# Optimization experiments

Measured on AMD Instinct MI355X. Metric: run time of the kernel, lower is better.

The kernel has to match this reference:

```python
import jax, jax.numpy as jnp
import numpy as np

B, T, N, H, DK = 4, 16, 256, 8, 64

def setup_inputs() -> dict:
    key = jax.random.key(0)
    k1, k2, k3 = jax.random.split(key, 3)
    queries = jax.random.normal(k1, (B, T, N, H, DK), dtype=jnp.float32)
    keys = jax.random.normal(k2, (B, T, N, H, DK), dtype=jnp.float32)
    values = jax.random.normal(k3, (B, T, N, H, DK), dtype=jnp.float32)
    attention_mask = jnp.zeros((B, T, 1, N, N), dtype=bool)  # unused: mask_flag=False
    return {"queries": queries, "keys": keys, "values": values, "attention_mask": attention_mask}

def reference(queries, keys, values, attention_mask):
    # queries: B T N H d_k; keys/values: B T S H d_k/d_v
    d_k = queries.shape[-1]
    scale = 1.0 / jnp.sqrt(jnp.asarray(d_k, queries.dtype))
    # scores: B T H N S
    scores = jnp.einsum('btnhe,btshe->bthns', queries, keys)
    # mask_flag=False -> no masking; dropout is identity in eval mode
    A = jax.nn.softmax(scale * scores, axis=-1)
    V = jnp.einsum('bthns,btshd->btnhd', A, values)
    return V
```

## Files before the change

kernel.cpp:

```cpp
#include <hip/hip_runtime.h>


typedef short short8 __attribute__((ext_vector_type(8)));
typedef float floatx4 __attribute__((ext_vector_type(4)));

__device__ __forceinline__ unsigned cvt_pk(float lo, float hi) {
  unsigned r;
  asm("v_cvt_pk_bf16_f32 %0, %1, %2" : "=v"(r) : "v"(lo), "v"(hi));
  return r;
}

constexpr int KSTR = 72;
constexpr int VSTR = 264;

__global__ __launch_bounds__(512, 4) void attn_kernel(
    const float* __restrict__ Q, const float* __restrict__ K,
    const float* __restrict__ V, float* __restrict__ O) {
  __shared__ __align__(16) short Klds[256 * KSTR];
  __shared__ __align__(16) short Vt[64 * VSTR];

  const int inst = blockIdx.x;
  const int h    = inst & 7;
  const int bt   = inst >> 3;
  const int base = bt * (256 * 512) + h * 64;
  const int tid  = threadIdx.x;

  {
    const float* Kb = K + base;
    #pragma unroll
    for (int i = 0; i < 8; ++i) {
      int idx = i * 512 + tid;
      int s = idx >> 4, c4 = idx & 15;
      float4 v = *reinterpret_cast<const float4*>(Kb + s * 512 + c4 * 4);
      uint2 w;
      w.x = cvt_pk(v.x, v.y);
      w.y = cvt_pk(v.z, v.w);
      *reinterpret_cast<uint2*>(&Klds[s * KSTR + c4 * 4]) = w;
    }
  }
  {
    const float* Vb = V + base;
    unsigned* Vt32 = reinterpret_cast<unsigned*>(Vt);
    #pragma unroll
    for (int i = 0; i < 4; ++i) {
      int idx = i * 512 + tid;
      int sp = idx >> 4, c4 = idx & 15;
      int s = sp * 2;
      float4 v0 = *reinterpret_cast<const float4*>(Vb + s * 512 + c4 * 4);
      float4 v1 = *reinterpret_cast<const float4*>(Vb + (s + 1) * 512 + c4 * 4);
      #pragma unroll
      for (int k = 0; k < 4; ++k) {
        Vt32[(c4 * 4 + k) * (VSTR / 2) + sp] = cvt_pk((&v0.x)[k], (&v1.x)[k]);
      }
    }
  }

  const int wave  = tid >> 6;
  const int lane  = tid & 63;
  const int c     = lane & 15;
  const int g     = lane >> 4;
  const int ghalf = (g & 1) * 32;
  const int gsel  = g >> 1;

  const float SCQ = 0.125f * 1.4426950408889634f;
  short8 qf[2][2];
  #pragma unroll
  for (int pass = 0; pass < 2; ++pass) {
    #pragma unroll
    for (int ks2 = 0; ks2 < 2; ++ks2) {
      const float* qp =
          Q + base + (pass * 128 + wave * 16 + c) * 512 + ks2 * 32 + g * 8;
      float4 a = *reinterpret_cast<const float4*>(qp);
      float4 b = *reinterpret_cast<const float4*>(qp + 4);
      union { unsigned u[4]; short8 s; } t;
      t.u[0] = cvt_pk(a.x * SCQ, a.y * SCQ);
      t.u[1] = cvt_pk(a.z * SCQ, a.w * SCQ);
      t.u[2] = cvt_pk(b.x * SCQ, b.y * SCQ);
      t.u[3] = cvt_pk(b.z * SCQ, b.w * SCQ);
      qf[pass][ks2] = t.s;
    }
  }
  __syncthreads();

  #pragma unroll
  for (int pass = 0; pass < 2; ++pass) {
    const int n0 = pass * 128 + wave * 16;

    floatx4 ao[4];
    #pragma unroll
    for (int dt = 0; dt < 4; ++dt) ao[dt] = floatx4{0.f, 0.f, 0.f, 0.f};
    float ps0 = 0.f, ps1 = 0.f, ps2 = 0.f, ps3 = 0.f;

    #pragma unroll
    for (int ks = 0; ks < 8; ++ks) {
      unsigned pk2[2][2];
      #pragma unroll
      for (int tt = 0; tt < 2; ++tt) {
        const int t = 2 * ks + tt;
        floatx4 acc = {0.f, 0.f, 0.f, 0.f};
        #pragma unroll
        for (int ks2 = 0; ks2 < 2; ++ks2) {
          short8 kf = *reinterpret_cast<const short8*>(
              &Klds[(t * 16 + c) * KSTR + ks2 * 32 + g * 8]);
          acc = __builtin_amdgcn_mfma_f32_16x16x32_bf16(kf, qf[pass][ks2], acc,
                                                        0, 0, 0);
        }
        float e0 = exp2f(acc[0]);
        float e1 = exp2f(acc[1]);
        float e2 = exp2f(acc[2]);
        float e3 = exp2f(acc[3]);
        ps0 += e0; ps1 += e1; ps2 += e2; ps3 += e3;
        pk2[tt][0] = cvt_pk(e0, e1);
        pk2[tt][1] = cvt_pk(e2, e3);
      }

      unsigned a0 = __shfl(pk2[0][0], ghalf + c);
      unsigned a1 = __shfl(pk2[0][1], ghalf + c);
      unsigned a2 = __shfl(pk2[0][0], ghalf + 16 + c);
      unsigned a3 = __shfl(pk2[0][1], ghalf + 16 + c);
      unsigned b0 = __shfl(pk2[1][0], ghalf + c);
      unsigned b1 = __shfl(pk2[1][1], ghalf + c);
      unsigned b2 = __shfl(pk2[1][0], ghalf + 16 + c);
      unsigned b3 = __shfl(pk2[1][1], ghalf + 16 + c);
      union { unsigned u[4]; short8 s; } pa;
      pa.u[0] = gsel ? b0 : a0;
      pa.u[1] = gsel ? b1 : a1;
      pa.u[2] = gsel ? b2 : a2;
      pa.u[3] = gsel ? b3 : a3;

      #pragma unroll
      for (int dt = 0; dt < 4; ++dt) {
        short8 vf = *reinterpret_cast<const short8*>(
            &Vt[(dt * 16 + c) * VSTR + ks * 32 + g * 8]);
        ao[dt] = __builtin_amdgcn_mfma_f32_16x16x32_bf16(pa.s, vf, ao[dt],
                                                         0, 0, 0);
      }
    }

    float sum = (ps0 + ps1) + (ps2 + ps3);
    sum += __shfl_xor(sum, 16);
    sum += __shfl_xor(sum, 32);
    const float rcp = __builtin_amdgcn_rcpf(sum);
    float rcpv[4];
    #pragma unroll
    for (int r = 0; r < 4; ++r) rcpv[r] = __shfl(rcp, 4 * g + r);

    #pragma unroll
    for (int dt = 0; dt < 4; ++dt)
      #pragma unroll
      for (int r = 0; r < 4; ++r)
        O[base + (n0 + 4 * g + r) * 512 + dt * 16 + c] = ao[dt][r] * rcpv[r];
  }
}

extern "C" void kernel_launch(void* const* d_in, const int* in_sizes, int n_in,
                              void* d_out, int out_size, void* d_ws, size_t ws_size,
                              hipStream_t stream) {
  const float* Q = (const float*)d_in[0];
  const float* K = (const float*)d_in[1];
  const float* V = (const float*)d_in[2];
  float* O = (float*)d_out;
  attn_kernel<<<dim3(512), dim3(512), 0, stream>>>(Q, K, V, O);
}
```

Measured before the change: 32.24 us.

## Fuse both query passes to share K/V LDS fragments and use permlane swaps

The two sequential query passes are merged into one key loop that processes both 16-row query tiles together. Each K and V fragment read from LDS now feeds two MFMAs instead of one, which halves LDS traffic. The eight ds_bpermute shuffles and selects used to rebuild the P operand are replaced by v_permlane32_swap and v_permlane16_swap instructions. In exchange, accumulator and register pressure roughly doubles, which could cause spills or reduced occupancy under the 512x4 launch bounds.

```diff
diff --git a/kernel.cpp b/kernel.cpp
--- a/kernel.cpp
+++ b/kernel.cpp
@@ -55,21 +55,19 @@
     }
   }
 
-  const int wave  = tid >> 6;
-  const int lane  = tid & 63;
-  const int c     = lane & 15;
-  const int g     = lane >> 4;
-  const int ghalf = (g & 1) * 32;
-  const int gsel  = g >> 1;
+  const int wave = tid >> 6;
+  const int lane = tid & 63;
+  const int c    = lane & 15;
+  const int g    = lane >> 4;
 
   const float SCQ = 0.125f * 1.4426950408889634f;
   short8 qf[2][2];
   #pragma unroll
-  for (int pass = 0; pass < 2; ++pass) {
+  for (int p = 0; p < 2; ++p) {
     #pragma unroll
     for (int ks2 = 0; ks2 < 2; ++ks2) {
       const float* qp =
-          Q + base + (pass * 128 + wave * 16 + c) * 512 + ks2 * 32 + g * 8;
+          Q + base + (p * 128 + wave * 16 + c) * 512 + ks2 * 32 + g * 8;
       float4 a = *reinterpret_cast<const float4*>(qp);
       float4 b = *reinterpret_cast<const float4*>(qp + 4);
       union { unsigned u[4]; short8 s; } t;
@@ -77,79 +75,80 @@
       t.u[1] = cvt_pk(a.z * SCQ, a.w * SCQ);
       t.u[2] = cvt_pk(b.x * SCQ, b.y * SCQ);
       t.u[3] = cvt_pk(b.z * SCQ, b.w * SCQ);
-      qf[pass][ks2] = t.s;
+      qf[p][ks2] = t.s;
     }
   }
   __syncthreads();
 
+  floatx4 ao[2][4];
   #pragma unroll
-  for (int pass = 0; pass < 2; ++pass) {
-    const int n0 = pass * 128 + wave * 16;
+  for (int p = 0; p < 2; ++p)
+    #pragma unroll
+    for (int dt = 0; dt < 4; ++dt) ao[p][dt] = floatx4{0.f, 0.f, 0.f, 0.f};
+  float ps[2][4] = {{0.f, 0.f, 0.f, 0.f}, {0.f, 0.f, 0.f, 0.f}};
 
-    floatx4 ao[4];
+  #pragma unroll
+  for (int ks = 0; ks < 8; ++ks) {
+    unsigned pk2[2][2][2];
     #pragma unroll
-    for (int dt = 0; dt < 4; ++dt) ao[dt] = floatx4{0.f, 0.f, 0.f, 0.f};
-    float ps0 = 0.f, ps1 = 0.f, ps2 = 0.f, ps3 = 0.f;
-
-    #pragma unroll
-    for (int ks = 0; ks < 8; ++ks) {
-      unsigned pk2[2][2];
+    for (int tt = 0; tt < 2; ++tt) {
+      const int t = 2 * ks + tt;
+      short8 kf0 = *reinterpret_cast<const short8*>(
+          &Klds[(t * 16 + c) * KSTR + g * 8]);
+      short8 kf1 = *reinterpret_cast<const short8*>(
+          &Klds[(t * 16 + c) * KSTR + 32 + g * 8]);
       #pragma unroll
-      for (int tt = 0; tt < 2; ++tt) {
-        const int t = 2 * ks + tt;
+      for (int p = 0; p < 2; ++p) {
         floatx4 acc = {0.f, 0.f, 0.f, 0.f};
-        #pragma unroll
-        for (int ks2 = 0; ks2 < 2; ++ks2) {
-          short8 kf = *reinterpret_cast<const short8*>(
-              &Klds[(t * 16 + c) * KSTR + ks2 * 32 + g * 8]);
-          acc = __builtin_amdgcn_mfma_f32_16x16x32_bf16(kf, qf[pass][ks2], acc,
-                                                        0, 0, 0);
-        }
+        acc = __builtin_amdgcn_mfma_f32_16x16x32_bf16(kf0, qf[p][0], acc, 0, 0, 0);
+        acc = __builtin_amdgcn_mfma_f32_16x16x32_bf16(kf1, qf[p][1], acc, 0, 0, 0);
         float e0 = exp2f(acc[0]);
         float e1 = exp2f(acc[1]);
         float e2 = exp2f(acc[2]);
         float e3 = exp2f(acc[3]);
-        ps0 += e0; ps1 += e1; ps2 += e2; ps3 += e3;
-        pk2[tt][0] = cvt_pk(e0, e1);
-        pk2[tt][1] = cvt_pk(e2, e3);
-      }
-
-      unsigned a0 = __shfl(pk2[0][0], ghalf + c);
-      unsigned a1 = __shfl(pk2[0][1], ghalf + c);
-      unsigned a2 = __shfl(pk2[0][0], ghalf + 16 + c);
-      unsigned a3 = __shfl(pk2[0][1], ghalf + 16 + c);
-      unsigned b0 = __shfl(pk2[1][0], ghalf + c);
-      unsigned b1 = __shfl(pk2[1][1], ghalf + c);
-      unsigned b2 = __shfl(pk2[1][0], ghalf + 16 + c);
-      unsigned b3 = __shfl(pk2[1][1], ghalf + 16 + c);
-      union { unsigned u[4]; short8 s; } pa;
-      pa.u[0] = gsel ? b0 : a0;
-      pa.u[1] = gsel ? b1 : a1;
-      pa.u[2] = gsel ? b2 : a2;
-      pa.u[3] = gsel ? b3 : a3;
-
-      #pragma unroll
-      for (int dt = 0; dt < 4; ++dt) {
-        short8 vf = *reinterpret_cast<const short8*>(
-            &Vt[(dt * 16 + c) * VSTR + ks * 32 + g * 8]);
-        ao[dt] = __builtin_amdgcn_mfma_f32_16x16x32_bf16(pa.s, vf, ao[dt],
-                                                         0, 0, 0);
+        ps[p][0] += e0; ps[p][1] += e1; ps[p][2] += e2; ps[p][3] += e3;
+        pk2[p][tt][0] = cvt_pk(e0, e1);
+        pk2[p][tt][1] = cvt_pk(e2, e3);
       }
     }
 
-    float sum = (ps0 + ps1) + (ps2 + ps3);
+    union { unsigned u[4]; short8 s; } pa[2];
+    #pragma unroll
+    for (int p = 0; p < 2; ++p) {
+      #pragma unroll
+      for (int m = 0; m < 2; ++m) {
+        unsigned x = pk2[p][0][m], y = pk2[p][1][m];
+        asm("v_permlane32_swap_b32 %0, %1" : "+v"(x), "+v"(y));
+        asm("v_permlane16_swap_b32 %0, %1" : "+v"(x), "+v"(y));
+        pa[p].u[m]     = x;
+        pa[p].u[2 + m] = y;
+      }
+    }
+
+    #pragma unroll
+    for (int dt = 0; dt < 4; ++dt) {
+      short8 vf = *reinterpret_cast<const short8*>(
+          &Vt[(dt * 16 + c) * VSTR + ks * 32 + g * 8]);
+      ao[0][dt] = __builtin_amdgcn_mfma_f32_16x16x32_bf16(pa[0].s, vf, ao[0][dt], 0, 0, 0);
+      ao[1][dt] = __builtin_amdgcn_mfma_f32_16x16x32_bf16(pa[1].s, vf, ao[1][dt], 0, 0, 0);
+    }
+  }
+
+  #pragma unroll
+  for (int p = 0; p < 2; ++p) {
+    const int n0 = p * 128 + wave * 16;
+    float sum = (ps[p][0] + ps[p][1]) + (ps[p][2] + ps[p][3]);
     sum += __shfl_xor(sum, 16);
     sum += __shfl_xor(sum, 32);
     const float rcp = __builtin_amdgcn_rcpf(sum);
     float rcpv[4];
     #pragma unroll
     for (int r = 0; r < 4; ++r) rcpv[r] = __shfl(rcp, 4 * g + r);
-
     #pragma unroll
     for (int dt = 0; dt < 4; ++dt)
       #pragma unroll
       for (int r = 0; r < 4; ++r)
-        O[base + (n0 + 4 * g + r) * 512 + dt * 16 + c] = ao[dt][r] * rcpv[r];
+        O[base + (n0 + 4 * g + r) * 512 + dt * 16 + c] = ao[p][dt][r] * rcpv[r];
   }
 }
 
```

New measurement: 30.77 us. -4.6%, faster.
